# Kernel tuning notes

Hardware: AMD Instinct MI355X
Metric: run time of the kernel (lower is better)

## Reference

```python
import jax, jax.numpy as jnp
import numpy as np

N, M, D_IN, D_TXT, D_OUT, H = 4096, 1024, 512, 512, 512, 8
DH = D_OUT // H


def positional_encoding(n, dim):
    # Matches PositionalEncoding: freq = exp((arange(dim//2)/dim)*ln(10000)),
    # x = pos/freq -> [L, dim//2], interleave (sin, cos) pairs -> [L, dim].
    pos = jnp.arange(n, dtype=jnp.float32)
    freq = jnp.exp((jnp.arange(dim // 2, dtype=jnp.float32) / dim) * jnp.log(jnp.float32(10000.0)))
    x = pos[:, None] / freq  # [L, dim//2]
    pe = jnp.stack((jnp.sin(x), jnp.cos(x)), axis=-1)  # [L, dim//2, 2]
    return pe.reshape(n, dim)


def setup_inputs() -> dict:
    key = jax.random.key(0)
    k1, k2, k3, k4, k5, k6 = jax.random.split(key, 6)
    s = 0.02
    return {
        "video_features": jax.random.normal(k1, (N, D_IN), dtype=jnp.float32),
        "text_features": jax.random.normal(k2, (M, D_TXT), dtype=jnp.float32),
        "Wq": jax.random.normal(k3, (H, D_IN, DH), dtype=jnp.float32) * s,
        "Wk": jax.random.normal(k4, (H, D_TXT, DH), dtype=jnp.float32) * s,
        "Wv": jax.random.normal(k5, (H, D_TXT, DH), dtype=jnp.float32) * s,
        "Wout": jax.random.normal(k6, (D_OUT, D_IN), dtype=jnp.float32) * s,
    }


def reference(video_features, text_features, Wq, Wk, Wv, Wout):
    # Batched over heads instead of the original per-head Python loop (same math).
    Q = jnp.einsum('nd,hde->hne', video_features, Wq)   # [H, N, DH]
    K = jnp.einsum('md,hde->hme', text_features, Wk)    # [H, M, DH]
    V = jnp.einsum('md,hde->hme', text_features, Wv)    # [H, M, DH]
    energies = jnp.einsum('hne,hme->hnm', Q, K)         # no scaling in original
    att = jax.nn.softmax(energies, axis=-1)             # dropout omitted (eval mode)
    y = jnp.einsum('hnm,hme->hne', att, V)              # [H, N, DH]
    y = jnp.transpose(y, (1, 0, 2)).reshape(video_features.shape[0], -1)  # concat heads
    y = y @ Wout                                        # [N, D_IN]
    y = y + positional_encoding(y.shape[0], y.shape[1])
    return y
```

## Files before the change

kernel.cpp:

```cpp
#include <hip/hip_runtime.h>
#include <hip/hip_bf16.h>
#include <math.h>

#define N_TOK 4096
#define M_TOK 1024
#define DMODEL 512
#define NHEAD 8
#define DHEAD 64

typedef __attribute__((ext_vector_type(8))) short short8;
typedef __attribute__((ext_vector_type(4))) float f32x4;
typedef __attribute__((ext_vector_type(4))) float float4v;

static __device__ __forceinline__ short f2bf(float f) {
    union { float f; unsigned u; } v; v.f = f;
    unsigned r = v.u + 0x7fffu + ((v.u >> 16) & 1u);
    return (short)(r >> 16);
}

__global__ __launch_bounds__(256) void pack_kernel(
        const float* __restrict__ xv, const float* __restrict__ xt,
        const float* __restrict__ wq, const float* __restrict__ wk,
        const float* __restrict__ wv, const float* __restrict__ wo,
        short* __restrict__ xvb, short* __restrict__ xtb,
        short* __restrict__ wqb, short* __restrict__ wkb,
        short* __restrict__ wvb, short* __restrict__ wob) {
    int bid = blockIdx.x;
    int t = threadIdx.x;
    if (bid < 256) {
        __shared__ float lds[64][65];
        const float* src;
        short* dst;
        int srstride;
        int dr0, dc0;
        if (bid < 192) {
            int mat = bid >> 6;
            int hb = bid & 63;
            int h = hb >> 3, dt = hb & 7;
            const float* W = (mat == 0) ? wq : (mat == 1) ? wk : wv;
            src = W + (size_t)h * (DMODEL * DHEAD) + (size_t)(dt * 64) * DHEAD;
            srstride = DHEAD;
            dst = (mat == 0) ? wqb : (mat == 1) ? wkb : wvb;
            dr0 = h * 64;
            dc0 = dt * 64;
        } else {
            int b = bid - 192;
            int rt = b >> 3, ct = b & 7;
            src = wo + (size_t)(rt * 64) * DMODEL + ct * 64;
            srstride = DMODEL;
            dst = wob;
            dr0 = ct * 64;
            dc0 = rt * 64;
        }
        {
            int r = t >> 2, c0 = (t & 3) * 16;
            const float* s = src + (size_t)r * srstride + c0;
            #pragma unroll
            for (int j = 0; j < 4; j++) {
                float4v v = *(const float4v*)(s + j * 4);
                lds[r][c0 + j * 4 + 0] = v[0];
                lds[r][c0 + j * 4 + 1] = v[1];
                lds[r][c0 + j * 4 + 2] = v[2];
                lds[r][c0 + j * 4 + 3] = v[3];
            }
        }
        __syncthreads();
        {
            int outr = t >> 2, c0 = (t & 3) * 16;
            short8 o0, o1;
            #pragma unroll
            for (int j = 0; j < 8; j++) {
                o0[j] = f2bf(lds[c0 + j][outr]);
                o1[j] = f2bf(lds[c0 + 8 + j][outr]);
            }
            short* d = dst + (size_t)(dr0 + outr) * DMODEL + dc0 + c0;
            *(short8*)d = o0;
            *(short8*)(d + 8) = o1;
        }
        return;
    }
    int idx = (bid - 256) * 256 + t;
    int stride = (gridDim.x - 256) * 256;
    const int CXV = N_TOK * DMODEL / 8;
    const int CXT = M_TOK * DMODEL / 8;
    for (int c = idx; c < CXV; c += stride) {
        float4v f0 = *(const float4v*)&xv[c * 8];
        float4v f1 = *(const float4v*)&xv[c * 8 + 4];
        short8 o;
        #pragma unroll
        for (int j = 0; j < 4; j++) { o[j] = f2bf(f0[j]); o[j + 4] = f2bf(f1[j]); }
        *(short8*)&xvb[c * 8] = o;
    }
    for (int c = idx; c < CXT; c += stride) {
        float4v f0 = *(const float4v*)&xt[c * 8];
        float4v f1 = *(const float4v*)&xt[c * 8 + 4];
        short8 o;
        #pragma unroll
        for (int j = 0; j < 4; j++) { o[j] = f2bf(f0[j]); o[j + 4] = f2bf(f1[j]); }
        *(short8*)&xtb[c * 8] = o;
    }
}

template<typename EPI>
static __device__ __forceinline__ void gemm_body(const short* __restrict__ A,
                                                 const short* __restrict__ BT,
                                                 int m0, int n0, EPI epi) {
    __shared__ __align__(16) short As[64][72];
    __shared__ __align__(16) short Bs[64][72];
    int t = threadIdx.x;
    int lane = t & 63, w = t >> 6;
    int wr = w >> 1, wc = w & 1;
    int l15 = lane & 15, g = lane >> 4;

    int row = t >> 2, c0 = (t & 3) * 16;
    const short* gA = A + (size_t)(m0 + row) * DMODEL + c0;
    const short* gB = BT + (size_t)(n0 + row) * DMODEL + c0;

    short8 ra0 = *(const short8*)gA;
    short8 ra1 = *(const short8*)(gA + 8);
    short8 rb0 = *(const short8*)gB;
    short8 rb1 = *(const short8*)(gB + 8);

    f32x4 acc[2][2] = {};
    #pragma unroll
    for (int step = 0; step < DMODEL / 64; ++step) {
        *(short8*)&As[row][c0]     = ra0;
        *(short8*)&As[row][c0 + 8] = ra1;
        *(short8*)&Bs[row][c0]     = rb0;
        *(short8*)&Bs[row][c0 + 8] = rb1;
        __syncthreads();
        if (step < DMODEL / 64 - 1) {
            gA += 64; gB += 64;
            ra0 = *(const short8*)gA;
            ra1 = *(const short8*)(gA + 8);
            rb0 = *(const short8*)gB;
            rb1 = *(const short8*)(gB + 8);
        }
        #pragma unroll
        for (int ks = 0; ks < 2; ks++) {
            short8 a[2], b[2];
            #pragma unroll
            for (int fr = 0; fr < 2; fr++) a[fr] = *(short8*)&As[wr * 32 + fr * 16 + l15][ks * 32 + g * 8];
            #pragma unroll
            for (int fc = 0; fc < 2; fc++) b[fc] = *(short8*)&Bs[wc * 32 + fc * 16 + l15][ks * 32 + g * 8];
            #pragma unroll
            for (int fr = 0; fr < 2; fr++)
                #pragma unroll
                for (int fc = 0; fc < 2; fc++)
                    acc[fr][fc] = __builtin_amdgcn_mfma_f32_16x16x32_bf16(a[fr], b[fc], acc[fr][fc], 0, 0, 0);
        }
        __syncthreads();
    }
    #pragma unroll
    for (int fr = 0; fr < 2; fr++)
        #pragma unroll
        for (int fc = 0; fc < 2; fc++)
            #pragma unroll
            for (int r = 0; r < 4; r++) {
                int orow = m0 + wr * 32 + fr * 16 + g * 4 + r;
                int ocol = n0 + wc * 32 + fc * 16 + l15;
                epi(orow, ocol, acc[fr][fc][r]);
            }
}

__global__ __launch_bounds__(256) void gemmQKV(const short* __restrict__ xvb,
                                               const short* __restrict__ xtb,
                                               const short* __restrict__ wqb,
                                               const short* __restrict__ wkb,
                                               const short* __restrict__ wvb,
                                               short* __restrict__ qb,
                                               short* __restrict__ kbm,
                                               short* __restrict__ vbt) {
    int bx = blockIdx.x;
    int n0 = blockIdx.y * 64;
    if (bx < 64) {
        short* C = qb;
        gemm_body(xvb, wqb, bx * 64, n0,
                  [&](int row, int col, float v) { C[(size_t)row * DMODEL + col] = f2bf(v); });
    } else if (bx < 80) {
        short* C = kbm;
        gemm_body(xtb, wkb, (bx - 64) * 64, n0,
                  [&](int row, int col, float v) { C[(size_t)row * DMODEL + col] = f2bf(v); });
    } else {
        short* C = vbt;
        gemm_body(xtb, wvb, (bx - 80) * 64, n0,
                  [&](int row, int col, float v) { C[(size_t)col * M_TOK + row] = f2bf(v); });
    }
}

__global__ __launch_bounds__(256) void gemmOut(const short* __restrict__ A,
                                               const short* __restrict__ BT,
                                               float* __restrict__ Cout) {
    __shared__ float ifreq[256];
    ifreq[threadIdx.x] = __expf(-(float)threadIdx.x * (9.210340371976184f / 512.0f));
    __syncthreads();
    gemm_body(A, BT, blockIdx.x * 64, blockIdx.y * 64,
              [&](int row, int col, float v) {
                  float x = (float)row * ifreq[col >> 1];
                  float s, c;
                  __sincosf(x, &s, &c);
                  Cout[(size_t)row * DMODEL + col] = v + ((col & 1) ? c : s);
              });
}

__global__ __launch_bounds__(256) void attn_kernel(const short* __restrict__ Qb,
                                                   const short* __restrict__ Kb,
                                                   const short* __restrict__ VbT,
                                                   short* __restrict__ Yb) {
    __shared__ __align__(16) short Ks[64][72];
    __shared__ __align__(16) short Vt[64][72];
    __shared__ __align__(16) short Ps[4][16][72];

    int bid = blockIdx.x;
    int h = bid & 7;
    int n0 = (bid >> 3) * 64;
    int t = threadIdx.x;
    int lane = t & 63, w = t >> 6;
    int l15 = lane & 15, g = lane >> 4;

    int row = t >> 2, c0 = (t & 3) * 16;
    const short* gK = Kb + (size_t)row * DMODEL + h * DHEAD + c0;
    const short* gV = VbT + (size_t)(h * DHEAD + row) * M_TOK + c0;

    short8 k0 = *(const short8*)gK;
    short8 k1 = *(const short8*)(gK + 8);
    short8 v0 = *(const short8*)gV;
    short8 v1 = *(const short8*)(gV + 8);

    const short* qrow = Qb + (size_t)(n0 + w * 16 + l15) * DMODEL + h * DHEAD;
    short8 qa0 = *(const short8*)(qrow + g * 8);
    short8 qa1 = *(const short8*)(qrow + 32 + g * 8);

    f32x4 acc[4] = {};
    f32x4 rsum = {};

    for (int it = 0; it < 16; ++it) {
        *(short8*)&Ks[row][c0]     = k0;
        *(short8*)&Ks[row][c0 + 8] = k1;
        *(short8*)&Vt[row][c0]     = v0;
        *(short8*)&Vt[row][c0 + 8] = v1;
        __syncthreads();
        if (it < 15) {
            gK += (size_t)64 * DMODEL;
            gV += 64;
            k0 = *(const short8*)gK;
            k1 = *(const short8*)(gK + 8);
            v0 = *(const short8*)gV;
            v1 = *(const short8*)(gV + 8);
        }
        #pragma unroll
        for (int kt = 0; kt < 4; kt++) {
            short8 kf0 = *(short8*)&Ks[kt * 16 + l15][g * 8];
            short8 kf1 = *(short8*)&Ks[kt * 16 + l15][32 + g * 8];
            f32x4 e = {};
            e = __builtin_amdgcn_mfma_f32_16x16x32_bf16(qa0, kf0, e, 0, 0, 0);
            e = __builtin_amdgcn_mfma_f32_16x16x32_bf16(qa1, kf1, e, 0, 0, 0);
            #pragma unroll
            for (int r = 0; r < 4; r++) {
                float p = exp2f(e[r] * 1.44269504f);
                rsum[r] += p;
                Ps[w][g * 4 + r][kt * 16 + l15] = f2bf(p);
            }
        }
        #pragma unroll
        for (int kb2 = 0; kb2 < 2; kb2++) {
            short8 pa = *(short8*)&Ps[w][l15][kb2 * 32 + g * 8];
            #pragma unroll
            for (int nt = 0; nt < 4; nt++) {
                short8 vf = *(short8*)&Vt[nt * 16 + l15][kb2 * 32 + g * 8];
                acc[nt] = __builtin_amdgcn_mfma_f32_16x16x32_bf16(pa, vf, acc[nt], 0, 0, 0);
            }
        }
        __syncthreads();
    }

    #pragma unroll
    for (int r = 0; r < 4; r++) {
        float s = rsum[r];
        s += __shfl_xor(s, 1);
        s += __shfl_xor(s, 2);
        s += __shfl_xor(s, 4);
        s += __shfl_xor(s, 8);
        rsum[r] = s;
    }

    #pragma unroll
    for (int nt = 0; nt < 4; nt++)
        #pragma unroll
        for (int r = 0; r < 4; r++) {
            float y = acc[nt][r] / rsum[r];
            Yb[(size_t)(n0 + w * 16 + g * 4 + r) * DMODEL + h * DHEAD + nt * 16 + l15] = f2bf(y);
        }
}

extern "C" void kernel_launch(void* const* d_in, const int* in_sizes, int n_in,
                              void* d_out, int out_size, void* d_ws, size_t ws_size,
                              hipStream_t stream) {
    const float* xv = (const float*)d_in[0];
    const float* xt = (const float*)d_in[1];
    const float* wq = (const float*)d_in[2];
    const float* wk = (const float*)d_in[3];
    const float* wv = (const float*)d_in[4];
    const float* wo = (const float*)d_in[5];

    short* xvb = (short*)d_ws;
    short* xtb = xvb + N_TOK * DMODEL;
    short* wqb = xtb + M_TOK * DMODEL;
    short* wkb = wqb + DMODEL * DMODEL;
    short* wvb = wkb + DMODEL * DMODEL;
    short* wob = wvb + DMODEL * DMODEL;
    short* qb  = wob + DMODEL * DMODEL;
    short* kbm = qb  + N_TOK * DMODEL;
    short* vbt = kbm + M_TOK * DMODEL;
    short* yb  = vbt + M_TOK * DMODEL;

    pack_kernel<<<1280, 256, 0, stream>>>(xv, xt, wq, wk, wv, wo,
                                          xvb, xtb, wqb, wkb, wvb, wob);
    gemmQKV<<<dim3(96, 8), 256, 0, stream>>>(xvb, xtb, wqb, wkb, wvb, qb, kbm, vbt);
    attn_kernel<<<512, 256, 0, stream>>>(qb, kbm, vbt, yb);
    gemmOut<<<dim3(64, 8), 256, 0, stream>>>(yb, wob, (float*)d_out);
}
```

Before: 58.75 us.

## Split attention key range across two wave groups and merge partial sums

The attention kernel now runs 512 threads per block. Two groups of four waves each process half of the 1024 keys, so each block needs 8 iterations instead of 16. Partial output accumulators and row sums are merged through shared memory, which is unioned with the K/V/P tiles. The intent is more parallelism per block and a shorter serial loop, since only 512 blocks run on 256 CUs. The cost is a larger block footprint, an extra merge step with a barrier, and one group of waves sitting idle during the final normalisation and store.

```diff
diff --git a/kernel.cpp b/kernel.cpp
--- a/kernel.cpp
+++ b/kernel.cpp
@@ -203,44 +203,56 @@
               });
 }
 
-__global__ __launch_bounds__(256) void attn_kernel(const short* __restrict__ Qb,
+struct AttnS {
+    short Ks[2][64][72];
+    short Vt[2][64][72];
+    short Ps[8][16][72];
+};
+struct MergeS {
+    f32x4 macc[4][4][64];
+    f32x4 mrs[4][64];
+};
+union AttnU { AttnS a; MergeS m; };
+
+__global__ __launch_bounds__(512) void attn_kernel(const short* __restrict__ Qb,
                                                    const short* __restrict__ Kb,
                                                    const short* __restrict__ VbT,
                                                    short* __restrict__ Yb) {
-    __shared__ __align__(16) short Ks[64][72];
-    __shared__ __align__(16) short Vt[64][72];
-    __shared__ __align__(16) short Ps[4][16][72];
+    __shared__ __align__(16) AttnU u;
 
     int bid = blockIdx.x;
     int h = bid & 7;
     int n0 = (bid >> 3) * 64;
     int t = threadIdx.x;
     int lane = t & 63, w = t >> 6;
+    int qg = w & 3, kh = w >> 2;
     int l15 = lane & 15, g = lane >> 4;
 
-    int row = t >> 2, c0 = (t & 3) * 16;
-    const short* gK = Kb + (size_t)row * DMODEL + h * DHEAD + c0;
-    const short* gV = VbT + (size_t)(h * DHEAD + row) * M_TOK + c0;
+    int sh = t >> 8;
+    int tt = t & 255;
+    int row = tt >> 2, c0 = (tt & 3) * 16;
+    const short* gK = Kb + (size_t)(sh * 512 + row) * DMODEL + h * DHEAD + c0;
+    const short* gV = VbT + (size_t)(h * DHEAD + row) * M_TOK + sh * 512 + c0;
 
     short8 k0 = *(const short8*)gK;
     short8 k1 = *(const short8*)(gK + 8);
     short8 v0 = *(const short8*)gV;
     short8 v1 = *(const short8*)(gV + 8);
 
-    const short* qrow = Qb + (size_t)(n0 + w * 16 + l15) * DMODEL + h * DHEAD;
+    const short* qrow = Qb + (size_t)(n0 + qg * 16 + l15) * DMODEL + h * DHEAD;
     short8 qa0 = *(const short8*)(qrow + g * 8);
     short8 qa1 = *(const short8*)(qrow + 32 + g * 8);
 
     f32x4 acc[4] = {};
     f32x4 rsum = {};
 
-    for (int it = 0; it < 16; ++it) {
-        *(short8*)&Ks[row][c0]     = k0;
-        *(short8*)&Ks[row][c0 + 8] = k1;
-        *(short8*)&Vt[row][c0]     = v0;
-        *(short8*)&Vt[row][c0 + 8] = v1;
-        __syncthreads();
-        if (it < 15) {
+    for (int it = 0; it < 8; ++it) {
+        *(short8*)&u.a.Ks[sh][row][c0]     = k0;
+        *(short8*)&u.a.Ks[sh][row][c0 + 8] = k1;
+        *(short8*)&u.a.Vt[sh][row][c0]     = v0;
+        *(short8*)&u.a.Vt[sh][row][c0 + 8] = v1;
+        __syncthreads();
+        if (it < 7) {
             gK += (size_t)64 * DMODEL;
             gV += 64;
             k0 = *(const short8*)gK;
@@ -250,8 +262,8 @@
         }
         #pragma unroll
         for (int kt = 0; kt < 4; kt++) {
-            short8 kf0 = *(short8*)&Ks[kt * 16 + l15][g * 8];
-            short8 kf1 = *(short8*)&Ks[kt * 16 + l15][32 + g * 8];
+            short8 kf0 = *(short8*)&u.a.Ks[kh][kt * 16 + l15][g * 8];
+            short8 kf1 = *(short8*)&u.a.Ks[kh][kt * 16 + l15][32 + g * 8];
             f32x4 e = {};
             e = __builtin_amdgcn_mfma_f32_16x16x32_bf16(qa0, kf0, e, 0, 0, 0);
             e = __builtin_amdgcn_mfma_f32_16x16x32_bf16(qa1, kf1, e, 0, 0, 0);
@@ -259,38 +271,48 @@
             for (int r = 0; r < 4; r++) {
                 float p = exp2f(e[r] * 1.44269504f);
                 rsum[r] += p;
-                Ps[w][g * 4 + r][kt * 16 + l15] = f2bf(p);
+                u.a.Ps[w][g * 4 + r][kt * 16 + l15] = f2bf(p);
             }
         }
         #pragma unroll
         for (int kb2 = 0; kb2 < 2; kb2++) {
-            short8 pa = *(short8*)&Ps[w][l15][kb2 * 32 + g * 8];
+            short8 pa = *(short8*)&u.a.Ps[w][l15][kb2 * 32 + g * 8];
             #pragma unroll
             for (int nt = 0; nt < 4; nt++) {
-                short8 vf = *(short8*)&Vt[nt * 16 + l15][kb2 * 32 + g * 8];
+                short8 vf = *(short8*)&u.a.Vt[kh][nt * 16 + l15][kb2 * 32 + g * 8];
                 acc[nt] = __builtin_amdgcn_mfma_f32_16x16x32_bf16(pa, vf, acc[nt], 0, 0, 0);
             }
         }
         __syncthreads();
     }
 
-    #pragma unroll
-    for (int r = 0; r < 4; r++) {
-        float s = rsum[r];
-        s += __shfl_xor(s, 1);
-        s += __shfl_xor(s, 2);
-        s += __shfl_xor(s, 4);
-        s += __shfl_xor(s, 8);
-        rsum[r] = s;
-    }
-
-    #pragma unroll
-    for (int nt = 0; nt < 4; nt++)
+    if (kh == 1) {
+        #pragma unroll
+        for (int nt = 0; nt < 4; nt++) u.m.macc[qg][nt][lane] = acc[nt];
+        u.m.mrs[qg][lane] = rsum;
+    }
+    __syncthreads();
+    if (kh == 0) {
+        #pragma unroll
+        for (int nt = 0; nt < 4; nt++) acc[nt] += u.m.macc[qg][nt][lane];
+        rsum += u.m.mrs[qg][lane];
         #pragma unroll
         for (int r = 0; r < 4; r++) {
-            float y = acc[nt][r] / rsum[r];
-            Yb[(size_t)(n0 + w * 16 + g * 4 + r) * DMODEL + h * DHEAD + nt * 16 + l15] = f2bf(y);
-        }
+            float s = rsum[r];
+            s += __shfl_xor(s, 1);
+            s += __shfl_xor(s, 2);
+            s += __shfl_xor(s, 4);
+            s += __shfl_xor(s, 8);
+            rsum[r] = s;
+        }
+        #pragma unroll
+        for (int nt = 0; nt < 4; nt++)
+            #pragma unroll
+            for (int r = 0; r < 4; r++) {
+                float y = acc[nt][r] / rsum[r];
+                Yb[(size_t)(n0 + qg * 16 + g * 4 + r) * DMODEL + h * DHEAD + nt * 16 + l15] = f2bf(y);
+            }
+    }
 }
 
 extern "C" void kernel_launch(void* const* d_in, const int* in_sizes, int n_in,
@@ -317,6 +339,6 @@
     pack_kernel<<<1280, 256, 0, stream>>>(xv, xt, wq, wk, wv, wo,
                                           xvb, xtb, wqb, wkb, wvb, wob);
     gemmQKV<<<dim3(96, 8), 256, 0, stream>>>(xvb, xtb, wqb, wkb, wvb, qb, kbm, vbt);
-    attn_kernel<<<512, 256, 0, stream>>>(qb, kbm, vbt, yb);
+    attn_kernel<<<512, 512, 0, stream>>>(qb, kbm, vbt, yb);
     gemmOut<<<dim3(64, 8), 256, 0, stream>>>(yb, wob, (float*)d_out);
 }
```

New measurement: 53.75 us. 1.09x faster.
